# Performance work log

Measured on AMD Instinct MI355X. Metric: run time of the kernel, lower is better.

The kernel has to match this reference:

```python
import math
import jax, jax.numpy as jnp
import numpy as np

NUM_HEADS = 16
D_MODEL = 1024
D_HEAD = 64
D_SEQ = 2048
NUM_LAYERS = 24
BATCH = 2


def setup_inputs() -> dict:
    key = jax.random.key(0)
    ks = jax.random.split(key, 10)
    s = math.sqrt(0.02)
    residual = jax.random.normal(ks[0], (BATCH, D_SEQ, D_MODEL), dtype=jnp.float32)
    W_Q = jax.random.normal(ks[1], (NUM_HEADS, D_MODEL, D_HEAD), dtype=jnp.float32) * s
    W_K = jax.random.normal(ks[2], (NUM_HEADS, D_MODEL, D_HEAD), dtype=jnp.float32) * s
    W_V = jax.random.normal(ks[3], (NUM_HEADS, D_MODEL, D_HEAD), dtype=jnp.float32) * s
    W_O = jax.random.normal(ks[4], (NUM_HEADS * D_HEAD, D_MODEL), dtype=jnp.float32) * s
    W_O = W_O / math.sqrt(NUM_LAYERS)
    b_Q = jax.random.normal(ks[5], (NUM_HEADS, D_HEAD), dtype=jnp.float32) * s
    b_K = jax.random.normal(ks[6], (NUM_HEADS, D_HEAD), dtype=jnp.float32) * s
    b_V = jax.random.normal(ks[7], (NUM_HEADS, D_HEAD), dtype=jnp.float32) * s
    b_O = jax.random.normal(ks[8], (D_MODEL,), dtype=jnp.float32) * s
    return dict(residual=residual, W_Q=W_Q, W_K=W_K, W_V=W_V, W_O=W_O,
                b_Q=b_Q, b_K=b_K, b_V=b_V, b_O=b_O)


def reference(residual, W_Q, W_K, W_V, W_O, b_Q, b_K, b_V, b_O):
    # residual: [b, s, m]; W_{Q,K,V}: [h, m, d]; b_{Q,K,V}: [h, d]
    Q = jnp.einsum('hmd,bsm->bshd', W_Q, residual) + b_Q
    K = jnp.einsum('hmd,bsm->bshd', W_K, residual) + b_K
    V = jnp.einsum('hmd,bsm->bshd', W_V, residual) + b_V
    # full causal score matrix [b, h, s_q, s_k], masked with -inf above diagonal
    QK = jnp.einsum('bqhd,bkhd->bhqk', Q, K)
    seq = residual.shape[1]
    causal = jnp.triu(jnp.ones((seq, seq), dtype=bool), k=1)  # True above diag
    QK_masked = jnp.where(causal, -jnp.inf, QK)
    soft = jax.nn.softmax(QK_masked / math.sqrt(D_HEAD), axis=-1)
    attn = jnp.einsum('bhqk,bkhd->bqhd', soft, V)  # [b, s, h, d]
    multi_head = attn.reshape(attn.shape[0], attn.shape[1], NUM_HEADS * D_HEAD)
    return jnp.einsum('em,bqe->bqm', W_O, multi_head) + b_O
```

## Files before the change

kernel.cpp:

```cpp
#include <hip/hip_runtime.h>
#include <stdint.h>

typedef unsigned short u16;
typedef unsigned long long u64;
typedef _Float16 f16;
typedef __attribute__((ext_vector_type(8))) _Float16 f16x8;
typedef __attribute__((ext_vector_type(4))) float f32x4;
typedef __attribute__((ext_vector_type(16))) float f32x16;
typedef __attribute__((ext_vector_type(4))) unsigned short u16x4;
typedef __attribute__((ext_vector_type(8))) unsigned short u16x8;

#define NHEADS 16
#define DMODEL 1024
#define DHEAD 64
#define SEQ 2048
#define NBATCH 2
#define MROWS (NBATCH * SEQ)
#define NQKV 3072
#define SCQ 0.18033688011112042f

__device__ __forceinline__ u16 f2h(float x) {
  union { f16 h; u16 u; } v;
  v.h = (f16)x;
  return v.u;
}

__device__ __forceinline__ unsigned pk2u(float x, float y) {
  typedef __fp16 fp16x2 __attribute__((ext_vector_type(2)));
  fp16x2 h = __builtin_amdgcn_cvt_pkrtz(x, y);
  union { fp16x2 h; unsigned u; } v; v.h = h;
  return v.u;
}

__device__ __forceinline__ f16x8 mkfrag(unsigned w0, unsigned w1, unsigned w2, unsigned w3) {
  union { unsigned u[4]; f16x8 f; } t;
  t.u[0] = w0; t.u[1] = w1; t.u[2] = w2; t.u[3] = w3;
  return t.f;
}

__device__ __forceinline__ f16x8 vfrag(const char* row, int sz, int F, int hib8) {
  union { u64 u[2]; f16x8 f; } t;
  t.u[0] = *(const u64*)(row + (((2 * F) ^ sz) << 4) + hib8);
  t.u[1] = *(const u64*)(row + (((2 * F + 1) ^ sz) << 4) + hib8);
  return t.f;
}

__device__ __forceinline__ void gload_lds16(const void* g, void* l) {
  __builtin_amdgcn_global_load_lds(
      (const __attribute__((address_space(1))) void*)g,
      (__attribute__((address_space(3))) void*)l, 16, 0, 0);
}

__global__ __launch_bounds__(256) void prep_kernel(
    const float* __restrict__ X,
    const float* __restrict__ WQ, const float* __restrict__ WK,
    const float* __restrict__ WV, const float* __restrict__ WO,
    u16* __restrict__ Xh, u16* __restrict__ Wqkv, u16* __restrict__ Wo) {
  __shared__ u16 lt[64][72];
  int blk = blockIdx.x;
  if (blk < 2048) {
    int i = blk * 256 + threadIdx.x;
    const f32x4* xv = (const f32x4*)(X + (size_t)i * 8);
    f32x4 a = xv[0], b = xv[1];
    u16x8 o;
    o[0] = f2h(a[0]); o[1] = f2h(a[1]); o[2] = f2h(a[2]); o[3] = f2h(a[3]);
    o[4] = f2h(b[0]); o[5] = f2h(b[1]); o[6] = f2h(b[2]); o[7] = f2h(b[3]);
    *(u16x8*)(Xh + (size_t)i * 8) = o;
  } else if (blk < 2816) {
    int bb = blk - 2048;
    int mt = bb & 15, hh = (bb >> 4) & 15, qkv = bb >> 8;
    const float* W = (qkv == 0) ? WQ : (qkv == 1) ? WK : WV;
    int m_in = threadIdx.x >> 2, dq = threadIdx.x & 3;
    const f32x4* sp4 = (const f32x4*)(W + (size_t)hh * (DMODEL * DHEAD) +
                                      (size_t)(mt * 64 + m_in) * DHEAD + dq * 16);
#pragma unroll
    for (int v4 = 0; v4 < 4; ++v4) {
      f32x4 a = sp4[v4];
#pragma unroll
      for (int j = 0; j < 4; ++j) lt[dq * 16 + v4 * 4 + j][m_in] = f2h(a[j]);
    }
    __syncthreads();
    int d_in = threadIdx.x >> 2, mq = threadIdx.x & 3;
    size_t orow = ((size_t)(qkv * 1024 + hh * 64 + d_in)) * DMODEL + mt * 64 + mq * 16;
    u16x8 o0, o1;
#pragma unroll
    for (int j = 0; j < 8; ++j) {
      o0[j] = lt[d_in][mq * 16 + j];
      o1[j] = lt[d_in][mq * 16 + 8 + j];
    }
    *(u16x8*)(Wqkv + orow) = o0;
    *(u16x8*)(Wqkv + orow + 8) = o1;
  } else {
    int bb = blk - 2816;
    int mt = bb & 15, et = bb >> 4;
    int e_in = threadIdx.x >> 2, mq = threadIdx.x & 3;
    const f32x4* sp4 = (const f32x4*)(WO + (size_t)(et * 64 + e_in) * DMODEL + mt * 64 + mq * 16);
#pragma unroll
    for (int v4 = 0; v4 < 4; ++v4) {
      f32x4 a = sp4[v4];
#pragma unroll
      for (int j = 0; j < 4; ++j) lt[mq * 16 + v4 * 4 + j][e_in] = f2h(a[j]);
    }
    __syncthreads();
    int m_in = threadIdx.x >> 2, eq = threadIdx.x & 3;
    size_t orow = (size_t)(mt * 64 + m_in) * DMODEL + et * 64 + eq * 16;
    u16x8 o0, o1;
#pragma unroll
    for (int j = 0; j < 8; ++j) {
      o0[j] = lt[m_in][eq * 16 + j];
      o1[j] = lt[m_in][eq * 16 + 8 + j];
    }
    *(u16x8*)(Wo + orow) = o0;
    *(u16x8*)(Wo + orow + 8) = o1;
  }
}

__global__ __launch_bounds__(256, 2) void gemm_qkv(
    const u16* __restrict__ A, const u16* __restrict__ Bt,
    const float* __restrict__ bq, const float* __restrict__ bk, const float* __restrict__ bv,
    u16* __restrict__ Qo, u16* __restrict__ Ko, u16* __restrict__ Vto) {
  __shared__ u16 lds[2][8192];
  const int tid = threadIdx.x;
  const int wid = tid >> 6, lane = tid & 63, lr = lane & 15, lg = lane >> 4;
  const int wr = wid >> 1, wc = wid & 1;
  const int brow = blockIdx.y * 128, bcol = blockIdx.x * 128;

  f32x4 acc[4][4];
#pragma unroll
  for (int i = 0; i < 4; ++i)
#pragma unroll
    for (int j = 0; j < 4; ++j) acc[i][j] = (f32x4){0.f, 0.f, 0.f, 0.f};

#define STAGE(buf, kt)                                                               \
  {                                                                                  \
    _Pragma("unroll") for (int i = 0; i < 2; ++i) {                                  \
      int idx = tid + i * 256;                                                       \
      gload_lds16(A + (size_t)(brow + (idx >> 2)) * 1024 + (kt) * 32 + (idx & 3) * 8,\
                  (char*)&lds[buf][0] + (wid * 64 + i * 256) * 16);                  \
    }                                                                                \
    _Pragma("unroll") for (int i = 0; i < 2; ++i) {                                  \
      int idx = tid + i * 256;                                                       \
      gload_lds16(Bt + (size_t)(bcol + (idx >> 2)) * 1024 + (kt) * 32 + (idx & 3) * 8,\
                  (char*)&lds[buf][4096] + (wid * 64 + i * 256) * 16);               \
    }                                                                                \
  }

  STAGE(0, 0);
  __syncthreads();
  int cur = 0;
  for (int kt = 0; kt < 32; ++kt) {
    if (kt + 1 < 32) STAGE(cur ^ 1, kt + 1);
    const u16* Ab = &lds[cur][0];
    const u16* Bb = &lds[cur][4096];
    f16x8 a[4], b[4];
#pragma unroll
    for (int ar = 0; ar < 4; ++ar)
      a[ar] = *(const f16x8*)(Ab + (wr * 64 + ar * 16 + lr) * 32 + lg * 8);
#pragma unroll
    for (int bc = 0; bc < 4; ++bc)
      b[bc] = *(const f16x8*)(Bb + (wc * 64 + bc * 16 + lr) * 32 + lg * 8);
#pragma unroll
    for (int ar = 0; ar < 4; ++ar)
#pragma unroll
      for (int bc = 0; bc < 4; ++bc)
        acc[ar][bc] = __builtin_amdgcn_mfma_f32_16x16x32_f16(a[ar], b[bc], acc[ar][bc], 0, 0, 0);
    __syncthreads();
    cur ^= 1;
  }
#undef STAGE

#pragma unroll
  for (int ar = 0; ar < 4; ++ar) {
    int row0 = brow + wr * 64 + ar * 16 + lg * 4;
    int bb = row0 >> 11, s0 = row0 & 2047;
#pragma unroll
    for (int bc = 0; bc < 4; ++bc) {
      int n = bcol + wc * 64 + bc * 16 + lr;
      int qkv = n >> 10, hd = n & 1023, h = hd >> 6, d = hd & 63;
      float bias = ((qkv == 0) ? bq : (qkv == 1) ? bk : bv)[hd];
      if (qkv < 2) {
        u16* dst = qkv ? Ko : Qo;
        float sc = qkv ? 1.f : SCQ;
        size_t base = ((size_t)(bb * NHEADS + h) * SEQ + s0) * DHEAD + d;
#pragma unroll
        for (int r = 0; r < 4; ++r)
          dst[base + (size_t)r * DHEAD] = f2h((acc[ar][bc][r] + bias) * sc);
      } else {
        u16x4 o;
        o[0] = f2h(acc[ar][bc][0] + bias);
        o[1] = f2h(acc[ar][bc][1] + bias);
        o[2] = f2h(acc[ar][bc][2] + bias);
        o[3] = f2h(acc[ar][bc][3] + bias);
        *(u16x4*)(Vto + ((size_t)(bb * NHEADS + h) * DHEAD + d) * SEQ + s0) = o;
      }
    }
  }
}

__global__ __launch_bounds__(256, 2) void gemm_out(
    const u16* __restrict__ A, const u16* __restrict__ Bt,
    const float* __restrict__ bo, float* __restrict__ Co) {
  __shared__ u16 lds[2][6144];
  const int tid = threadIdx.x;
  const int wid = tid >> 6, lane = tid & 63, lr = lane & 15, lg = lane >> 4;
  const int wr = wid >> 1, wc = wid & 1;
  const int brow = blockIdx.y * 64, bcol = blockIdx.x * 128;

  f32x4 acc[2][4];
#pragma unroll
  for (int i = 0; i < 2; ++i)
#pragma unroll
    for (int j = 0; j < 4; ++j) acc[i][j] = (f32x4){0.f, 0.f, 0.f, 0.f};

#define OSTAGE(buf, kt)                                                              \
  {                                                                                  \
    {                                                                                \
      int idx = tid;                                                                 \
      gload_lds16(A + (size_t)(brow + (idx >> 2)) * 1024 + (kt) * 32 + (idx & 3) * 8,\
                  (char*)&lds[buf][0] + (wid * 64) * 16);                            \
    }                                                                                \
    _Pragma("unroll") for (int i = 0; i < 2; ++i) {                                  \
      int idx = tid + i * 256;                                                       \
      gload_lds16(Bt + (size_t)(bcol + (idx >> 2)) * 1024 + (kt) * 32 + (idx & 3) * 8,\
                  (char*)&lds[buf][2048] + (wid * 64 + i * 256) * 16);               \
    }                                                                                \
  }

  OSTAGE(0, 0);
  __syncthreads();
  int cur = 0;
  for (int kt = 0; kt < 32; ++kt) {
    if (kt + 1 < 32) OSTAGE(cur ^ 1, kt + 1);
    const u16* Ab = &lds[cur][0];
    const u16* Bb = &lds[cur][2048];
    f16x8 a[2], b[4];
#pragma unroll
    for (int ar = 0; ar < 2; ++ar)
      a[ar] = *(const f16x8*)(Ab + (wr * 32 + ar * 16 + lr) * 32 + lg * 8);
#pragma unroll
    for (int bc = 0; bc < 4; ++bc)
      b[bc] = *(const f16x8*)(Bb + (wc * 64 + bc * 16 + lr) * 32 + lg * 8);
#pragma unroll
    for (int ar = 0; ar < 2; ++ar)
#pragma unroll
      for (int bc = 0; bc < 4; ++bc)
        acc[ar][bc] = __builtin_amdgcn_mfma_f32_16x16x32_f16(a[ar], b[bc], acc[ar][bc], 0, 0, 0);
    __syncthreads();
    cur ^= 1;
  }
#undef OSTAGE

#pragma unroll
  for (int ar = 0; ar < 2; ++ar) {
    int row0 = brow + wr * 32 + ar * 16 + lg * 4;
#pragma unroll
    for (int bc = 0; bc < 4; ++bc) {
      int n = bcol + wc * 64 + bc * 16 + lr;
      float bias = bo[n];
#pragma unroll
      for (int r = 0; r < 4; ++r)
        Co[(size_t)(row0 + r) * DMODEL + n] = acc[ar][bc][r] + bias;
    }
  }
}

__global__ __launch_bounds__(256, 2) void attn_kernel(
    const u16* __restrict__ Q, const u16* __restrict__ K,
    const u16* __restrict__ Vt, u16* __restrict__ MH) {
  __shared__ char sh8[32768];
  const int tid = threadIdx.x, wid = tid >> 6, lane = tid & 63;
  const int l31 = lane & 31, hi = lane >> 5;
  const int pairid = wid >> 1;
  const int qsub = wid & 1;
  const int bid = blockIdx.x;
  const int qidx = bid >> 5, bh = bid & 31;
  const int t = (qidx < 8) ? (31 - qidx) : (qidx < 16) ? (qidx - 8)
              : (qidx < 24) ? (39 - qidx) : (qidx - 16);
  const int h = bh & 15, b = bh >> 4;
  const u16* Qb = Q + (size_t)bh * (SEQ * DHEAD);
  const u16* Kb = K + (size_t)bh * (SEQ * DHEAD);
  const u16* Vb = Vt + (size_t)bh * (DHEAD * SEQ);

  const int sw0 = (l31 ^ (l31 >> 3)) & 7, kz0 = sw0 << 4;
  const int r32 = 32 + l31;
  const int sw1 = (r32 ^ (r32 >> 3)) & 7, kz1 = sw1 << 4;
  const int hib = hi * 16, hib8 = hi * 8;

#pragma unroll
  for (int i = 0; i < 2; ++i) {
    int idx = tid + i * 256, row = idx >> 3;
    int sseg = (idx & 7) ^ ((row ^ (row >> 3)) & 7);
    gload_lds16(Qb + (size_t)(t * 64 + row) * DHEAD + sseg * 8, sh8 + 16384 + idx * 16);
    gload_lds16(Kb + (size_t)row * DHEAD + sseg * 8, sh8 + idx * 16);
    if (t >= 1)
      gload_lds16(Kb + (size_t)(64 + row) * DHEAD + sseg * 8, sh8 + 8192 + idx * 16);
  }
  __syncthreads();

  f16x8 qf0, qf1, qf2, qf3;
  {
    int row = (qsub << 5) + l31;
    int swz = ((row ^ (row >> 3)) & 7) << 4;
    const char* qb = sh8 + 16384 + row * 128;
    qf0 = *(const f16x8*)(qb + ((hib + 0)  ^ swz));
    qf1 = *(const f16x8*)(qb + ((hib + 32) ^ swz));
    qf2 = *(const f16x8*)(qb + ((hib + 64) ^ swz));
    qf3 = *(const f16x8*)(qb + ((hib + 96) ^ swz));
  }
  __syncthreads();

#pragma unroll
  for (int i = 0; i < 2; ++i) {
    int idx = tid + i * 256, row = idx >> 3;
    int sseg = (idx & 7) ^ ((row ^ (row >> 3)) & 7);
    gload_lds16(Vb + (size_t)row * SEQ + sseg * 8, sh8 + 16384 + idx * 16);
    if (t >= 1)
      gload_lds16(Vb + (size_t)row * SEQ + 64 + sseg * 8, sh8 + 24576 + idx * 16);
  }

  f32x16 acc0, acc1;
#pragma unroll
  for (int z = 0; z < 16; ++z) { acc0[z] = 0.f; acc1[z] = 0.f; }
  float m = -1e30f, l = 0.f;
  const int qg = t * 64 + (qsub << 5) + l31;
  const int wall = (t >> 1) + 1;

  for (int si = 0; si < wall; ++si) {
    const int kt = 2 * si + pairid;
    const bool act = (kt <= t);
    f16x8 pa0, pa1, pa2, pa3;

    if (act) {
      const char* kbuf = sh8 + pairid * 8192;

      f32x16 s0, s1;
#pragma unroll
      for (int z = 0; z < 16; ++z) { s0[z] = 0.f; s1[z] = 0.f; }
      {
        const char* kb0 = kbuf + l31 * 128;
        const char* kb1 = kbuf + r32 * 128;
        f16x8 kf;
        __builtin_amdgcn_s_setprio(1);
        kf = *(const f16x8*)(kb0 + ((hib + 0)  ^ kz0)); s0 = __builtin_amdgcn_mfma_f32_32x32x16_f16(kf, qf0, s0, 0, 0, 0);
        kf = *(const f16x8*)(kb0 + ((hib + 32) ^ kz0)); s0 = __builtin_amdgcn_mfma_f32_32x32x16_f16(kf, qf1, s0, 0, 0, 0);
        kf = *(const f16x8*)(kb0 + ((hib + 64) ^ kz0)); s0 = __builtin_amdgcn_mfma_f32_32x32x16_f16(kf, qf2, s0, 0, 0, 0);
        kf = *(const f16x8*)(kb0 + ((hib + 96) ^ kz0)); s0 = __builtin_amdgcn_mfma_f32_32x32x16_f16(kf, qf3, s0, 0, 0, 0);
        kf = *(const f16x8*)(kb1 + ((hib + 0)  ^ kz1)); s1 = __builtin_amdgcn_mfma_f32_32x32x16_f16(kf, qf0, s1, 0, 0, 0);
        kf = *(const f16x8*)(kb1 + ((hib + 32) ^ kz1)); s1 = __builtin_amdgcn_mfma_f32_32x32x16_f16(kf, qf1, s1, 0, 0, 0);
        kf = *(const f16x8*)(kb1 + ((hib + 64) ^ kz1)); s1 = __builtin_amdgcn_mfma_f32_32x32x16_f16(kf, qf2, s1, 0, 0, 0);
        kf = *(const f16x8*)(kb1 + ((hib + 96) ^ kz1)); s1 = __builtin_amdgcn_mfma_f32_32x32x16_f16(kf, qf3, s1, 0, 0, 0);
        __builtin_amdgcn_s_setprio(0);
      }

      if (kt == t) {
#pragma unroll
        for (int rr = 0; rr < 16; ++rr) {
          int k0 = kt * 64 + (rr & 3) + 8 * (rr >> 2) + 4 * hi;
          if (k0 > qg) s0[rr] = -1e30f;
          if (k0 + 32 > qg) s1[rr] = -1e30f;
        }
      }

      float tm = s0[0];
#pragma unroll
      for (int rr = 1; rr < 16; ++rr) tm = fmaxf(tm, s0[rr]);
#pragma unroll
      for (int rr = 0; rr < 16; ++rr) tm = fmaxf(tm, s1[rr]);
      tm = fmaxf(tm, __shfl_xor(tm, 32));

      if (!__all(tm <= m + 8.f)) {
        float m2 = fmaxf(m, tm);
        float al = exp2f(m - m2);
        m = m2;
        l *= al;
#pragma unroll
        for (int rr = 0; rr < 16; ++rr) {
          int qp = (rr & 3) + 8 * (rr >> 2) + 4 * hi;
          float af = __shfl(al, qp);
          acc0[rr] *= af;
          acc1[rr] *= af;
        }
      }

      float rs = 0.f;
#pragma unroll
      for (int rr = 0; rr < 16; ++rr) { s0[rr] = exp2f(s0[rr] - m); rs += s0[rr]; }
#pragma unroll
      for (int rr = 0; rr < 16; ++rr) { s1[rr] = exp2f(s1[rr] - m); rs += s1[rr]; }
      rs += __shfl_xor(rs, 32);
      l += rs;

      pa0 = mkfrag(pk2u(s0[0],  s0[1]),  pk2u(s0[2],  s0[3]),
                   pk2u(s0[4],  s0[5]),  pk2u(s0[6],  s0[7]));
      pa1 = mkfrag(pk2u(s0[8],  s0[9]),  pk2u(s0[10], s0[11]),
                   pk2u(s0[12], s0[13]), pk2u(s0[14], s0[15]));
      pa2 = mkfrag(pk2u(s1[0],  s1[1]),  pk2u(s1[2],  s1[3]),
                   pk2u(s1[4],  s1[5]),  pk2u(s1[6],  s1[7]));
      pa3 = mkfrag(pk2u(s1[8],  s1[9]),  pk2u(s1[10], s1[11]),
                   pk2u(s1[12], s1[13]), pk2u(s1[14], s1[15]));
    }

    __syncthreads();

    const int e = 2 * si + 2;
    if (e <= t) {
#pragma unroll
      for (int i = 0; i < 2; ++i) {
        int idx = tid + i * 256, row = idx >> 3;
        int sseg = (idx & 7) ^ ((row ^ (row >> 3)) & 7);
        gload_lds16(Kb + (size_t)(e * 64 + row) * DHEAD + sseg * 8, sh8 + idx * 16);
        if (e + 1 <= t)
          gload_lds16(Kb + (size_t)((e + 1) * 64 + row) * DHEAD + sseg * 8,
                      sh8 + 8192 + idx * 16);
      }
    }

    if (act) {
      const char* vbuf = sh8 + 16384 + pairid * 8192;
      const char* vr0 = vbuf + l31 * 128;
      const char* vr1 = vbuf + r32 * 128;
      __builtin_amdgcn_s_setprio(1);
      acc0 = __builtin_amdgcn_mfma_f32_32x32x16_f16(pa0, vfrag(vr0, sw0, 0, hib8), acc0, 0, 0, 0);
      acc0 = __builtin_amdgcn_mfma_f32_32x32x16_f16(pa1, vfrag(vr0, sw0, 1, hib8), acc0, 0, 0, 0);
      acc0 = __builtin_amdgcn_mfma_f32_32x32x16_f16(pa2, vfrag(vr0, sw0, 2, hib8), acc0, 0, 0, 0);
      acc0 = __builtin_amdgcn_mfma_f32_32x32x16_f16(pa3, vfrag(vr0, sw0, 3, hib8), acc0, 0, 0, 0);
      acc1 = __builtin_amdgcn_mfma_f32_32x32x16_f16(pa0, vfrag(vr1, sw1, 0, hib8), acc1, 0, 0, 0);
      acc1 = __builtin_amdgcn_mfma_f32_32x32x16_f16(pa1, vfrag(vr1, sw1, 1, hib8), acc1, 0, 0, 0);
      acc1 = __builtin_amdgcn_mfma_f32_32x32x16_f16(pa2, vfrag(vr1, sw1, 2, hib8), acc1, 0, 0, 0);
      acc1 = __builtin_amdgcn_mfma_f32_32x32x16_f16(pa3, vfrag(vr1, sw1, 3, hib8), acc1, 0, 0, 0);
      __builtin_amdgcn_s_setprio(0);
    }

    __syncthreads();

    if (e <= t) {
#pragma unroll
      for (int i = 0; i < 2; ++i) {
        int idx = tid + i * 256, row = idx >> 3;
        int sseg = (idx & 7) ^ ((row ^ (row >> 3)) & 7);
        gload_lds16(Vb + (size_t)row * SEQ + e * 64 + sseg * 8, sh8 + 16384 + idx * 16);
        if (e + 1 <= t)
          gload_lds16(Vb + (size_t)row * SEQ + (e + 1) * 64 + sseg * 8,
                      sh8 + 24576 + idx * 16);
      }
    }
  }

  {
    const int slot = (qsub << 6) | (hi << 5) | l31;
    float* z = (float*)(sh8 + (pairid ? 16384 : 0)) + slot * 18;
    z[0] = m; z[1] = l;
#pragma unroll
    for (int rr = 0; rr < 16; ++rr) z[2 + rr] = pairid ? acc0[rr] : acc1[rr];
    __syncthreads();
    const float* y = (const float*)(sh8 + (pairid ? 0 : 16384)) + slot * 18;
    float mb = y[0], lb = y[1];
    float mM = fmaxf(m, mb);
    float aw = exp2f(m - mM), bw = exp2f(mb - mM);
    float lM = l * aw + lb * bw;
    const int d = pairid ? (32 + l31) : l31;
#pragma unroll
    for (int rr = 0; rr < 16; ++rr) {
      int qp = (rr & 3) + 8 * (rr >> 2) + 4 * hi;
      float aF = __shfl(aw, qp), bF = __shfl(bw, qp), lF = __shfl(lM, qp);
      float own = pairid ? acc1[rr] : acc0[rr];
      float val = (own * aF + y[2 + rr] * bF) / lF;
      int q = t * 64 + (qsub << 5) + qp;
      MH[((size_t)(b * SEQ) + q) * DMODEL + h * DHEAD + d] = f2h(val);
    }
  }
}

extern "C" void kernel_launch(void* const* d_in, const int* in_sizes, int n_in,
                              void* d_out, int out_size, void* d_ws, size_t ws_size,
                              hipStream_t stream) {
  const float* residual = (const float*)d_in[0];
  const float* WQ = (const float*)d_in[1];
  const float* WK = (const float*)d_in[2];
  const float* WV = (const float*)d_in[3];
  const float* WO = (const float*)d_in[4];
  const float* bQ = (const float*)d_in[5];
  const float* bK = (const float*)d_in[6];
  const float* bV = (const float*)d_in[7];
  const float* bO = (const float*)d_in[8];
  float* out = (float*)d_out;

  char* w = (char*)d_ws;
  u16* Xh   = (u16*)(w);
  u16* Wqkv = (u16*)(w + ((size_t)8 << 20));
  u16* Wo   = (u16*)(w + ((size_t)14 << 20));
  u16* Qd   = (u16*)(w + ((size_t)16 << 20));
  u16* Kd   = (u16*)(w + ((size_t)24 << 20));
  u16* Vtd  = (u16*)(w + ((size_t)32 << 20));
  u16* MH   = (u16*)(w + ((size_t)40 << 20));

  prep_kernel<<<3072, 256, 0, stream>>>(residual, WQ, WK, WV, WO, Xh, Wqkv, Wo);

  gemm_qkv<<<dim3(NQKV / 128, MROWS / 128), 256, 0, stream>>>(
      Xh, Wqkv, bQ, bK, bV, Qd, Kd, Vtd);

  attn_kernel<<<1024, 256, 0, stream>>>(Qd, Kd, Vtd, MH);

  gemm_out<<<dim3(DMODEL / 128, MROWS / 64), 256, 0, stream>>>(MH, Wo, bO, out);
}
```

Measured before the change: 111.5 us.

## Split long causal attention tiles across two blocks and merge partials

Query tiles 16-31, the ones with the longest causal key ranges, are each split into two halves of key tiles handled by separate blocks, guided by a lookup table that orders the work longest-first. Split blocks write unnormalised partial outputs plus the running max and sum to a float workspace. A new merge kernel combines the two halves and writes the final fp16 output. This aims to cut the tail imbalance of the causal grid, at the cost of an extra kernel launch and extra global traffic for the partials.

```diff
diff --git a/kernel.cpp b/kernel.cpp
--- a/kernel.cpp
+++ b/kernel.cpp
@@ -50,6 +50,13 @@
       (const __attribute__((address_space(1))) void*)g,
       (__attribute__((address_space(3))) void*)l, 16, 0, 0);
 }
+
+__device__ const unsigned char JT[48] = {
+   95, 127,  94, 126,  93, 125,  92,  15,  14,
+  124,  91, 123,  90, 122,  89, 121,  88,  13,  12,
+  120,  87, 119,  86, 118,  85, 117,  84,  11,  10,
+  116,  83, 115,  82, 114,  81, 113,  80,   9,   8,
+  112,   7,   6,   5,   4,   3,   2,   1,   0 };
 
 __global__ __launch_bounds__(256) void prep_kernel(
     const float* __restrict__ X,
@@ -266,16 +273,23 @@
 
 __global__ __launch_bounds__(256, 2) void attn_kernel(
     const u16* __restrict__ Q, const u16* __restrict__ K,
-    const u16* __restrict__ Vt, u16* __restrict__ MH) {
+    const u16* __restrict__ Vt, u16* __restrict__ MH, float* __restrict__ PP) {
   __shared__ char sh8[32768];
   const int tid = threadIdx.x, wid = tid >> 6, lane = tid & 63;
   const int l31 = lane & 31, hi = lane >> 5;
   const int pairid = wid >> 1;
   const int qsub = wid & 1;
   const int bid = blockIdx.x;
-  const int qidx = bid >> 5, bh = bid & 31;
-  const int t = (qidx < 8) ? (31 - qidx) : (qidx < 16) ? (qidx - 8)
-              : (qidx < 24) ? (39 - qidx) : (qidx - 16);
+  const int j = bid >> 5, bh = bid & 31;
+  const unsigned en = JT[j];
+  const int t = en & 31;
+  const int half = (en >> 5) & 1;
+  const int split = en >> 6;
+  const int nk = t + 1;
+  const int nA = (nk + 1) >> 1;
+  const int kbeg = (split && half) ? nA : 0;
+  const int kcnt = split ? (half ? nk - nA : nA) : nk;
+  const int wall = (kcnt + 1) >> 1;
   const int h = bh & 15, b = bh >> 4;
   const u16* Qb = Q + (size_t)bh * (SEQ * DHEAD);
   const u16* Kb = K + (size_t)bh * (SEQ * DHEAD);
@@ -291,9 +305,9 @@
     int idx = tid + i * 256, row = idx >> 3;
     int sseg = (idx & 7) ^ ((row ^ (row >> 3)) & 7);
     gload_lds16(Qb + (size_t)(t * 64 + row) * DHEAD + sseg * 8, sh8 + 16384 + idx * 16);
-    gload_lds16(Kb + (size_t)row * DHEAD + sseg * 8, sh8 + idx * 16);
-    if (t >= 1)
-      gload_lds16(Kb + (size_t)(64 + row) * DHEAD + sseg * 8, sh8 + 8192 + idx * 16);
+    gload_lds16(Kb + (size_t)((kbeg) * 64 + row) * DHEAD + sseg * 8, sh8 + idx * 16);
+    if (kcnt > 1)
+      gload_lds16(Kb + (size_t)((kbeg + 1) * 64 + row) * DHEAD + sseg * 8, sh8 + 8192 + idx * 16);
   }
   __syncthreads();
 
@@ -313,9 +327,9 @@
   for (int i = 0; i < 2; ++i) {
     int idx = tid + i * 256, row = idx >> 3;
     int sseg = (idx & 7) ^ ((row ^ (row >> 3)) & 7);
-    gload_lds16(Vb + (size_t)row * SEQ + sseg * 8, sh8 + 16384 + idx * 16);
-    if (t >= 1)
-      gload_lds16(Vb + (size_t)row * SEQ + 64 + sseg * 8, sh8 + 24576 + idx * 16);
+    gload_lds16(Vb + (size_t)row * SEQ + kbeg * 64 + sseg * 8, sh8 + 16384 + idx * 16);
+    if (kcnt > 1)
+      gload_lds16(Vb + (size_t)row * SEQ + (kbeg + 1) * 64 + sseg * 8, sh8 + 24576 + idx * 16);
   }
 
   f32x16 acc0, acc1;
@@ -323,11 +337,11 @@
   for (int z = 0; z < 16; ++z) { acc0[z] = 0.f; acc1[z] = 0.f; }
   float m = -1e30f, l = 0.f;
   const int qg = t * 64 + (qsub << 5) + l31;
-  const int wall = (t >> 1) + 1;
 
   for (int si = 0; si < wall; ++si) {
-    const int kt = 2 * si + pairid;
-    const bool act = (kt <= t);
+    const int ktl = 2 * si + pairid;
+    const bool act = (ktl < kcnt);
+    const int gkt = kbeg + ktl;
     f16x8 pa0, pa1, pa2, pa3;
 
     if (act) {
@@ -352,10 +366,10 @@
         __builtin_amdgcn_s_setprio(0);
       }
 
-      if (kt == t) {
+      if (gkt == t) {
 #pragma unroll
         for (int rr = 0; rr < 16; ++rr) {
-          int k0 = kt * 64 + (rr & 3) + 8 * (rr >> 2) + 4 * hi;
+          int k0 = gkt * 64 + (rr & 3) + 8 * (rr >> 2) + 4 * hi;
           if (k0 > qg) s0[rr] = -1e30f;
           if (k0 + 32 > qg) s1[rr] = -1e30f;
         }
@@ -402,15 +416,15 @@
 
     __syncthreads();
 
-    const int e = 2 * si + 2;
-    if (e <= t) {
+    const int el = 2 * si + 2;
+    if (el < kcnt) {
 #pragma unroll
       for (int i = 0; i < 2; ++i) {
         int idx = tid + i * 256, row = idx >> 3;
         int sseg = (idx & 7) ^ ((row ^ (row >> 3)) & 7);
-        gload_lds16(Kb + (size_t)(e * 64 + row) * DHEAD + sseg * 8, sh8 + idx * 16);
-        if (e + 1 <= t)
-          gload_lds16(Kb + (size_t)((e + 1) * 64 + row) * DHEAD + sseg * 8,
+        gload_lds16(Kb + (size_t)((kbeg + el) * 64 + row) * DHEAD + sseg * 8, sh8 + idx * 16);
+        if (el + 1 < kcnt)
+          gload_lds16(Kb + (size_t)((kbeg + el + 1) * 64 + row) * DHEAD + sseg * 8,
                       sh8 + 8192 + idx * 16);
       }
     }
@@ -433,14 +447,14 @@
 
     __syncthreads();
 
-    if (e <= t) {
+    if (el < kcnt) {
 #pragma unroll
       for (int i = 0; i < 2; ++i) {
         int idx = tid + i * 256, row = idx >> 3;
         int sseg = (idx & 7) ^ ((row ^ (row >> 3)) & 7);
-        gload_lds16(Vb + (size_t)row * SEQ + e * 64 + sseg * 8, sh8 + 16384 + idx * 16);
-        if (e + 1 <= t)
-          gload_lds16(Vb + (size_t)row * SEQ + (e + 1) * 64 + sseg * 8,
+        gload_lds16(Vb + (size_t)row * SEQ + (kbeg + el) * 64 + sseg * 8, sh8 + 16384 + idx * 16);
+        if (el + 1 < kcnt)
+          gload_lds16(Vb + (size_t)row * SEQ + (kbeg + el + 1) * 64 + sseg * 8,
                       sh8 + 24576 + idx * 16);
       }
     }
@@ -459,15 +473,52 @@
     float aw = exp2f(m - mM), bw = exp2f(mb - mM);
     float lM = l * aw + lb * bw;
     const int d = pairid ? (32 + l31) : l31;
-#pragma unroll
-    for (int rr = 0; rr < 16; ++rr) {
-      int qp = (rr & 3) + 8 * (rr >> 2) + 4 * hi;
-      float aF = __shfl(aw, qp), bF = __shfl(bw, qp), lF = __shfl(lM, qp);
-      float own = pairid ? acc1[rr] : acc0[rr];
-      float val = (own * aF + y[2 + rr] * bF) / lF;
-      int q = t * 64 + (qsub << 5) + qp;
-      MH[((size_t)(b * SEQ) + q) * DMODEL + h * DHEAD + d] = f2h(val);
-    }
+    if (!split) {
+#pragma unroll
+      for (int rr = 0; rr < 16; ++rr) {
+        int qp = (rr & 3) + 8 * (rr >> 2) + 4 * hi;
+        float aF = __shfl(aw, qp), bF = __shfl(bw, qp), lF = __shfl(lM, qp);
+        float own = pairid ? acc1[rr] : acc0[rr];
+        float val = (own * aF + y[2 + rr] * bF) / lF;
+        int q = t * 64 + (qsub << 5) + qp;
+        MH[((size_t)(b * SEQ) + q) * DMODEL + h * DHEAD + d] = f2h(val);
+      }
+    } else {
+      float* wsb = PP + ((size_t)((bh << 4) | (t - 16)) * 2 + half) * (64 * 66);
+#pragma unroll
+      for (int rr = 0; rr < 16; ++rr) {
+        int qp = (rr & 3) + 8 * (rr >> 2) + 4 * hi;
+        float aF = __shfl(aw, qp), bF = __shfl(bw, qp);
+        float own = pairid ? acc1[rr] : acc0[rr];
+        wsb[((qsub << 5) + qp) * 66 + d] = own * aF + y[2 + rr] * bF;
+      }
+      if (pairid == 0 && hi == 0) {
+        wsb[((qsub << 5) + l31) * 66 + 64] = mM;
+        wsb[((qsub << 5) + l31) * 66 + 65] = lM;
+      }
+    }
+  }
+}
+
+__global__ __launch_bounds__(256) void attn_merge(const float* __restrict__ PP,
+                                                  u16* __restrict__ MH) {
+  const int tile = blockIdx.x;
+  const int bh = tile >> 4, t = (tile & 15) + 16;
+  const int h = bh & 15, b = bh >> 4;
+  const int d = threadIdx.x & 63, rg = threadIdx.x >> 6;
+  const float* A = PP + (size_t)(tile * 2 + 0) * (64 * 66);
+  const float* B = PP + (size_t)(tile * 2 + 1) * (64 * 66);
+#pragma unroll
+  for (int i = 0; i < 16; ++i) {
+    int row = rg * 16 + i;
+    float mA = A[row * 66 + 64], lA = A[row * 66 + 65];
+    float mB = B[row * 66 + 64], lB = B[row * 66 + 65];
+    float mM = fmaxf(mA, mB);
+    float wA = exp2f(mA - mM), wB = exp2f(mB - mM);
+    float lM = lA * wA + lB * wB;
+    float v = (A[row * 66 + d] * wA + B[row * 66 + d] * wB) / lM;
+    int q = t * 64 + row;
+    MH[((size_t)(b * SEQ) + q) * DMODEL + h * DHEAD + d] = f2h(v);
   }
 }
 
@@ -493,13 +544,15 @@
   u16* Kd   = (u16*)(w + ((size_t)24 << 20));
   u16* Vtd  = (u16*)(w + ((size_t)32 << 20));
   u16* MH   = (u16*)(w + ((size_t)40 << 20));
+  float* PP = (float*)(w + ((size_t)48 << 20));
 
   prep_kernel<<<3072, 256, 0, stream>>>(residual, WQ, WK, WV, WO, Xh, Wqkv, Wo);
 
   gemm_qkv<<<dim3(NQKV / 128, MROWS / 128), 256, 0, stream>>>(
       Xh, Wqkv, bQ, bK, bV, Qd, Kd, Vtd);
 
-  attn_kernel<<<1024, 256, 0, stream>>>(Qd, Kd, Vtd, MH);
+  attn_kernel<<<1536, 256, 0, stream>>>(Qd, Kd, Vtd, MH, PP);
+  attn_merge<<<512, 256, 0, stream>>>(PP, MH);
 
   gemm_out<<<dim3(DMODEL / 128, MROWS / 64), 256, 0, stream>>>(MH, Wo, bO, out);
 }
```

New measurement: 117.8 us. +5.7%, slower.
